# Performance work log

Hardware: AMD Instinct MI355X
Metric: run time of the kernel (lower is better)

## Reference

```python
import jax, jax.numpy as jnp
import numpy as np
from jax import lax

E = 18; I = 36; NH = 2; DHM = I // NH; DHS = E // NH; K = 4; S = 48; B = 4096
FF = 64  # multiple_of=64 rounding of 18*1.3

def _ln(x, w, eps=1e-5):
    mu = jnp.mean(x, axis=-1, keepdims=True)
    var = jnp.var(x, axis=-1, keepdims=True)
    return (x - mu) / jnp.sqrt(var + eps) * w

def _causal_conv(x, w, b):
    # x: (B,S,C); depthwise causal conv, w: (C,K), b: (C,)
    kk = w.shape[-1]
    xp = jnp.pad(x, ((0, 0), (kk - 1, 0), (0, 0)))
    y = lax.conv_general_dilated(xp, w[:, None, :], (1,), 'VALID',
                                 dimension_numbers=('NWC', 'OIW', 'NWC'),
                                 feature_group_count=x.shape[-1])
    return y + b

def _headwise(x, w):
    # block-diagonal linear (LinearHeadwiseExpand): w (n, dout, din)
    n, do, di = w.shape
    xr = x.reshape(x.shape[0], x.shape[1], n, di)
    return jnp.einsum('bsnd,nod->bsno', xr, w).reshape(x.shape[0], x.shape[1], n * do)

def _mlstm_parallel(q, k, v, ipre, fpre):
    # parallel_stabilized_simple: q,k,v (B,NH,S,DH); ipre,fpre (B,NH,S)
    dh = q.shape[-1]
    s = q.shape[2]
    lfc = jnp.cumsum(jax.nn.log_sigmoid(fpre), axis=-1)            # (B,NH,S)
    dlog = lfc[..., :, None] - lfc[..., None, :]                   # (B,NH,S,S): t,s
    mask = jnp.tril(jnp.ones((s, s), dtype=bool))
    logD = jnp.where(mask, dlog + ipre[..., None, :], -jnp.inf)
    maxD = jnp.max(logD, axis=-1, keepdims=True)
    D = jnp.exp(logD - maxD)
    qk = jnp.einsum('bhsd,bhtd->bhst', q, k * (dh ** -0.5))
    C = qk * D
    norm = jnp.maximum(jnp.abs(jnp.sum(C, axis=-1, keepdims=True)), jnp.exp(-maxD))
    return jnp.einsum('bhst,bhtd->bhsd', C / (norm + 1e-6), v)

def _mlstm_block(x, ln_w, up_w, cw, cb, qw, kw, vw, igw, igb, fgw, fgb, skip, onw, dw):
    bsz, s = x.shape[0], x.shape[1]
    h = _ln(x, ln_w)
    up = h @ up_w                                                  # (B,S,2I)
    xm, z = up[..., :I], up[..., I:]
    xc = jax.nn.silu(_causal_conv(xm, cw, cb))
    q = _headwise(xc, qw); k = _headwise(xc, kw); v = _headwise(xm, vw)
    gin = jnp.concatenate([q, k, v], axis=-1)                      # (B,S,3I)
    ipre = jnp.einsum('bsf,hf->bhs', gin, igw) + igb[None, :, None]
    fpre = jnp.einsum('bsf,hf->bhs', gin, fgw) + fgb[None, :, None]
    hd = lambda t: t.reshape(bsz, s, NH, DHM).transpose(0, 2, 1, 3)
    ht = _mlstm_parallel(hd(q), hd(k), hd(v), ipre, fpre)          # (B,NH,S,DHM)
    mu = jnp.mean(ht, axis=-1, keepdims=True)
    var = jnp.var(ht, axis=-1, keepdims=True)
    hn = (ht - mu) / jnp.sqrt(var + 1e-5) * onw.reshape(NH, DHM)[None, :, None, :]
    hn = hn.transpose(0, 2, 1, 3).reshape(bsz, s, I)
    hst = (hn + skip * xc) * jax.nn.silu(z)
    return x + hst @ dw

def _slstm_block(x, ln_w, cw, cb, gw, rw, gb, gnw, fln_w, fup_w, fdn_w):
    bsz, s = x.shape[0], x.shape[1]
    h = _ln(x, ln_w)
    hc = jax.nn.silu(_causal_conv(h, cw, cb))
    def gate(inp, w):
        return jnp.einsum('bsnd,nod->bsno', inp.reshape(bsz, s, NH, DHS), w)
    # gate order: i, f (from conv), z, o (from raw)
    wx = jnp.stack([gate(hc, gw[0]), gate(hc, gw[1]), gate(h, gw[2]), gate(h, gw[3])], axis=2)  # (B,S,4,NH,DHS)
    z0 = jnp.zeros((bsz, NH, DHS), x.dtype)
    def step(carry, wx_t):
        y, c, n, m = carry
        raw = wx_t + jnp.einsum('bhd,hdge->bghe', y, rw) + gb[None]  # (B,4,NH,DHS)
        i_, f_, z_, o_ = raw[:, 0], raw[:, 1], raw[:, 2], raw[:, 3]
        lfm = m + jax.nn.log_sigmoid(f_)
        mn = jnp.maximum(i_, lfm)
        ig = jnp.exp(i_ - mn)
        fg = jnp.exp(lfm - mn)
        cn = fg * c + ig * jnp.tanh(z_)
        nn = fg * n + ig
        yn = jax.nn.sigmoid(o_) * cn / nn
        return (yn, cn, nn, mn), yn
    _, ys = lax.scan(step, (z0, z0, z0, z0), wx.transpose(1, 0, 2, 3, 4))
    y = ys.transpose(1, 0, 2, 3)                                   # (B,S,NH,DHS)
    mu = jnp.mean(y, axis=-1, keepdims=True)
    var = jnp.var(y, axis=-1, keepdims=True)
    y = (y - mu) / jnp.sqrt(var + 1e-5) * gnw.reshape(NH, DHS)[None, None]
    x = x + y.reshape(bsz, s, E)
    h2 = _ln(x, fln_w)
    u = h2 @ fup_w                                                 # (B,S,2*FF)
    g, upp = u[..., :FF], u[..., FF:]
    return x + (jax.nn.gelu(g, approximate=False) * upp) @ fdn_w

def reference(x, m_ln_w, m_up_w, m_conv_w, m_conv_b, m_q_w, m_k_w, m_v_w,
              m_ig_w, m_ig_b, m_fg_w, m_fg_b, m_skip, m_on_w, m_down_w,
              s_ln_w, s_conv_w, s_conv_b, s_gate_w, s_rec_w, s_bias, s_gn_w,
              f_ln_w, f_up_w, f_down_w, post_ln_w, dense_w, dense_b):
    mj = 0
    for blk in range(7):
        if blk == 1:  # slstm_at=[1]
            x = _slstm_block(x, s_ln_w, s_conv_w, s_conv_b, s_gate_w, s_rec_w,
                             s_bias, s_gn_w, f_ln_w, f_up_w, f_down_w)
        else:
            x = _mlstm_block(x, m_ln_w[mj], m_up_w[mj], m_conv_w[mj], m_conv_b[mj],
                             m_q_w[mj], m_k_w[mj], m_v_w[mj], m_ig_w[mj], m_ig_b[mj],
                             m_fg_w[mj], m_fg_b[mj], m_skip[mj], m_on_w[mj], m_down_w[mj])
            mj += 1
    x = _ln(x, post_ln_w)
    out = x @ dense_w + dense_b
    return out.at[:, :24, :].set(0.0)

def setup_inputs():
    key = jax.random.key(0)
    ks = jax.random.split(key, 24)
    r = lambda i, shp, sc=0.1: jax.random.normal(ks[i], shp, dtype=jnp.float32) * sc
    return {
        'x': jax.random.normal(ks[0], (B, S, E), dtype=jnp.float32),
        'm_ln_w': jnp.ones((6, E), jnp.float32),
        'm_up_w': r(1, (6, E, 2 * I)),
        'm_conv_w': r(2, (6, I, K)),
        'm_conv_b': r(3, (6, I)),
        'm_q_w': r(4, (6, 9, 4, 4)),
        'm_k_w': r(5, (6, 9, 4, 4)),
        'm_v_w': r(6, (6, 9, 4, 4)),
        'm_ig_w': r(7, (6, NH, 3 * I)),
        'm_ig_b': r(8, (6, NH)),
        'm_fg_w': r(9, (6, NH, 3 * I)),
        'm_fg_b': r(10, (6, NH)),
        'm_skip': r(11, (6, I)),
        'm_on_w': jnp.ones((6, I), jnp.float32),
        'm_down_w': r(12, (6, I, E)),
        's_ln_w': jnp.ones((E,), jnp.float32),
        's_conv_w': r(13, (E, K)),
        's_conv_b': r(14, (E,)),
        's_gate_w': r(15, (4, NH, DHS, DHS)),
        's_rec_w': r(16, (NH, DHS, 4, DHS)),
        's_bias': r(17, (4, NH, DHS)),
        's_gn_w': jnp.ones((E,), jnp.float32),
        'f_ln_w': jnp.ones((E,), jnp.float32),
        'f_up_w': r(18, (E, 2 * FF)),
        'f_down_w': r(19, (FF, E)),
        'post_ln_w': jnp.ones((E,), jnp.float32),
        'dense_w': r(20, (E, 1)),
        'dense_b': r(21, (1,)),
    }
```

## Files before the change

### kernel.cpp

```cpp
#include <hip/hip_runtime.h>
#include <math.h>

#define TPB 256
#define WPB 4

constexpr int WAVE_F = 3552;
constexpr int O_SZ   = 2688;

constexpr int OW_UP  = 0;
constexpr int OW_AB  = 7776;
constexpr int OW_FUP = 9504;

__device__ __forceinline__ float sigm(float v){ return 1.f/(1.f+__expf(-v)); }
__device__ __forceinline__ float siluf(float v){ return v/(1.f+__expf(-v)); }
__device__ __forceinline__ float logsig(float v){ return fminf(v,0.f) - log1pf(__expf(-fabsf(v))); }
__device__ __forceinline__ float sqf(float v){ return v*v; }
__device__ __forceinline__ unsigned short f2b(float v){
  union{float f; unsigned u;} c; c.f=v; unsigned u=c.u;
  return (unsigned short)((u + 0x7FFFu + ((u>>16)&1u))>>16);
}
__device__ __forceinline__ float b2f(unsigned short s){
  union{unsigned u; float f;} c; c.u=((unsigned)s)<<16; return c.f;
}
__device__ __forceinline__ float u2f(unsigned u){
  union{unsigned u; float f;} c; c.u=u; return c.f;
}
__device__ __forceinline__ unsigned packbf(float a, float b){
  return (unsigned)f2b(a) | ((unsigned)f2b(b)<<16);
}
__device__ __forceinline__ float dot4(const float4 a, const float4 b){
  return a.x*b.x+a.y*b.y+a.z*b.z+a.w*b.w;
}

struct V18 { float4 a,b,c,d; float2 e; };
struct V36 { float4 g0,g1,g2,g3,g4,g5,g6,g7,g8; };

template<int I> __device__ __forceinline__ float elc(const V18& v){
  if constexpr(I==0) return v.a.x; else if constexpr(I==1) return v.a.y;
  else if constexpr(I==2) return v.a.z; else if constexpr(I==3) return v.a.w;
  else if constexpr(I==4) return v.b.x; else if constexpr(I==5) return v.b.y;
  else if constexpr(I==6) return v.b.z; else if constexpr(I==7) return v.b.w;
  else if constexpr(I==8) return v.c.x; else if constexpr(I==9) return v.c.y;
  else if constexpr(I==10) return v.c.z; else if constexpr(I==11) return v.c.w;
  else if constexpr(I==12) return v.d.x; else if constexpr(I==13) return v.d.y;
  else if constexpr(I==14) return v.d.z; else if constexpr(I==15) return v.d.w;
  else if constexpr(I==16) return v.e.x; else return v.e.y;
}
template<int I> __device__ __forceinline__ void setv(V18& v, float x){
  if constexpr(I==0) v.a.x=x; else if constexpr(I==1) v.a.y=x;
  else if constexpr(I==2) v.a.z=x; else if constexpr(I==3) v.a.w=x;
  else if constexpr(I==4) v.b.x=x; else if constexpr(I==5) v.b.y=x;
  else if constexpr(I==6) v.b.z=x; else if constexpr(I==7) v.b.w=x;
  else if constexpr(I==8) v.c.x=x; else if constexpr(I==9) v.c.y=x;
  else if constexpr(I==10) v.c.z=x; else if constexpr(I==11) v.c.w=x;
  else if constexpr(I==12) v.d.x=x; else if constexpr(I==13) v.d.y=x;
  else if constexpr(I==14) v.d.z=x; else if constexpr(I==15) v.d.w=x;
  else if constexpr(I==16) v.e.x=x; else v.e.y=x;
}
template<int G> __device__ __forceinline__ float4& grp(V36& q){
  if constexpr(G==0) return q.g0; else if constexpr(G==1) return q.g1;
  else if constexpr(G==2) return q.g2; else if constexpr(G==3) return q.g3;
  else if constexpr(G==4) return q.g4; else if constexpr(G==5) return q.g5;
  else if constexpr(G==6) return q.g6; else if constexpr(G==7) return q.g7;
  else return q.g8;
}

__device__ __forceinline__ float dot18(const V18& h, const float* __restrict__ w){
  return h.a.x*w[0]+h.a.y*w[1]+h.a.z*w[2]+h.a.w*w[3]
       + h.b.x*w[4]+h.b.y*w[5]+h.b.z*w[6]+h.b.w*w[7]
       + h.c.x*w[8]+h.c.y*w[9]+h.c.z*w[10]+h.c.w*w[11]
       + h.d.x*w[12]+h.d.y*w[13]+h.d.z*w[14]+h.d.w*w[15]
       + h.e.x*w[16]+h.e.y*w[17];
}
__device__ __forceinline__ void axpy18(V18& x, float s, const float* __restrict__ w){
  x.a.x+=s*w[0];  x.a.y+=s*w[1];  x.a.z+=s*w[2];  x.a.w+=s*w[3];
  x.b.x+=s*w[4];  x.b.y+=s*w[5];  x.b.z+=s*w[6];  x.b.w+=s*w[7];
  x.c.x+=s*w[8];  x.c.y+=s*w[9];  x.c.z+=s*w[10]; x.c.w+=s*w[11];
  x.d.x+=s*w[12]; x.d.y+=s*w[13]; x.d.z+=s*w[14]; x.d.w+=s*w[15];
  x.e.x+=s*w[16]; x.e.y+=s*w[17];
}
template<int B> __device__ __forceinline__ float dot9(const V18& v, const float* __restrict__ w){
  return elc<B+0>(v)*w[0]+elc<B+1>(v)*w[1]+elc<B+2>(v)*w[2]+elc<B+3>(v)*w[3]
       + elc<B+4>(v)*w[4]+elc<B+5>(v)*w[5]+elc<B+6>(v)*w[6]+elc<B+7>(v)*w[7]
       + elc<B+8>(v)*w[8];
}

#define L18(M) M(0) M(1) M(2) M(3) M(4) M(5) M(6) M(7) M(8) M(9) M(10) M(11) M(12) M(13) M(14) M(15) M(16) M(17)
#define L9(M) M(0) M(1) M(2) M(3) M(4) M(5) M(6) M(7) M(8)

extern "C" __global__ void prep_kernel(
    const float* __restrict__ up,  const float* __restrict__ qw, const float* __restrict__ kw,
    const float* __restrict__ vw,  const float* __restrict__ igw,const float* __restrict__ fgw,
    const float* __restrict__ fup, float* __restrict__ W)
{
  const int tid = threadIdx.x;
  for (int i=tid;i<7776;i+=256){ int mj=i/1296, r=i%1296, o=r/18, d=r%18; W[OW_UP+i]=up[mj*1296+d*72+o]; }
  for (int i=tid;i<1728;i+=256){
    int mj=i/288, r=i%288, gh=r/72, w2=(r%72)/36, c=r%36;
    int g=gh>>1,h=gh&1,n=c>>2,d=c&3;
    const float* gwp=(g? fgw:igw)+mj*216+h*108;
    float val=0.f;
    if(w2==0){ for(int o=0;o<4;++o) val += qw[mj*144+n*16+o*4+d]*gwp[n*4+o] + kw[mj*144+n*16+o*4+d]*gwp[36+n*4+o]; }
    else     { for(int o=0;o<4;++o) val += vw[mj*144+n*16+o*4+d]*gwp[72+n*4+o]; }
    W[OW_AB+i]=val;
  }
  for (int i=tid;i<2304;i+=256){ int f=i/18, d=i%18; W[OW_FUP+i]=fup[d*128+f]; }
}

template<int G>
__device__ __forceinline__ void proj_g(const V18& h, V18& x, V36& q,
    float* kvrow, unsigned short* szrow, int lane,
    const float* __restrict__ wup, const float* __restrict__ wab,
    const float* __restrict__ cw,  const float* __restrict__ cb,
    const float* __restrict__ qw,  const float* __restrict__ kw, const float* __restrict__ vw,
    const float* __restrict__ skp, const float* __restrict__ dwn,
    float& gi0, float& gi1, float& gf0, float& gf1)
{
  constexpr int C0=4*G;
  float m0=dot18(h,wup+(C0+0)*18), m1=dot18(h,wup+(C0+1)*18),
        m2=dot18(h,wup+(C0+2)*18), m3=dot18(h,wup+(C0+3)*18);
  if(lane>=48){ m0=0.f;m1=0.f;m2=0.f;m3=0.f; }
  float c0,c1,c2,c3;
  { float p1=__shfl(m0,lane-1),p2=__shfl(m0,lane-2),p3=__shfl(m0,lane-3);
    c0=siluf(cb[C0+0]+p3*cw[(C0+0)*4]+p2*cw[(C0+0)*4+1]+p1*cw[(C0+0)*4+2]+m0*cw[(C0+0)*4+3]); }
  { float p1=__shfl(m1,lane-1),p2=__shfl(m1,lane-2),p3=__shfl(m1,lane-3);
    c1=siluf(cb[C0+1]+p3*cw[(C0+1)*4]+p2*cw[(C0+1)*4+1]+p1*cw[(C0+1)*4+2]+m1*cw[(C0+1)*4+3]); }
  { float p1=__shfl(m2,lane-1),p2=__shfl(m2,lane-2),p3=__shfl(m2,lane-3);
    c2=siluf(cb[C0+2]+p3*cw[(C0+2)*4]+p2*cw[(C0+2)*4+1]+p1*cw[(C0+2)*4+2]+m2*cw[(C0+2)*4+3]); }
  { float p1=__shfl(m3,lane-1),p2=__shfl(m3,lane-2),p3=__shfl(m3,lane-3);
    c3=siluf(cb[C0+3]+p3*cw[(C0+3)*4]+p2*cw[(C0+3)*4+1]+p1*cw[(C0+3)*4+2]+m3*cw[(C0+3)*4+3]); }
  const float s0=siluf(dot18(h,wup+(36+C0+0)*18));
  const float s1=siluf(dot18(h,wup+(36+C0+1)*18));
  const float s2=siluf(dot18(h,wup+(36+C0+2)*18));
  const float s3=siluf(dot18(h,wup+(36+C0+3)*18));
  gi0 += c0*wab[C0+0]+c1*wab[C0+1]+c2*wab[C0+2]+c3*wab[C0+3]
       + m0*wab[36+C0+0]+m1*wab[36+C0+1]+m2*wab[36+C0+2]+m3*wab[36+C0+3];
  gi1 += c0*wab[72+C0+0]+c1*wab[72+C0+1]+c2*wab[72+C0+2]+c3*wab[72+C0+3]
       + m0*wab[108+C0+0]+m1*wab[108+C0+1]+m2*wab[108+C0+2]+m3*wab[108+C0+3];
  gf0 += c0*wab[144+C0+0]+c1*wab[144+C0+1]+c2*wab[144+C0+2]+c3*wab[144+C0+3]
       + m0*wab[180+C0+0]+m1*wab[180+C0+1]+m2*wab[180+C0+2]+m3*wab[180+C0+3];
  gf1 += c0*wab[216+C0+0]+c1*wab[216+C0+1]+c2*wab[216+C0+2]+c3*wab[216+C0+3]
       + m0*wab[252+C0+0]+m1*wab[252+C0+1]+m2*wab[252+C0+2]+m3*wab[252+C0+3];
  if(lane<48){
    uint2 ss; ss.x=packbf(s0,s1); ss.y=packbf(s2,s3);
    *reinterpret_cast<uint2*>(reinterpret_cast<unsigned*>(szrow) + (C0>>1)) = ss;
    float4 kk;
    kk.x=c0*kw[G*16+0] +c1*kw[G*16+1] +c2*kw[G*16+2] +c3*kw[G*16+3];
    kk.y=c0*kw[G*16+4] +c1*kw[G*16+5] +c2*kw[G*16+6] +c3*kw[G*16+7];
    kk.z=c0*kw[G*16+8] +c1*kw[G*16+9] +c2*kw[G*16+10]+c3*kw[G*16+11];
    kk.w=c0*kw[G*16+12]+c1*kw[G*16+13]+c2*kw[G*16+14]+c3*kw[G*16+15];
    *reinterpret_cast<float4*>(kvrow + C0) = kk;
    float vt0=m0*vw[G*16+0] +m1*vw[G*16+1] +m2*vw[G*16+2] +m3*vw[G*16+3];
    float vt1=m0*vw[G*16+4] +m1*vw[G*16+5] +m2*vw[G*16+6] +m3*vw[G*16+7];
    float vt2=m0*vw[G*16+8] +m1*vw[G*16+9] +m2*vw[G*16+10]+m3*vw[G*16+11];
    float vt3=m0*vw[G*16+12]+m1*vw[G*16+13]+m2*vw[G*16+14]+m3*vw[G*16+15];
    unsigned* urow = reinterpret_cast<unsigned*>(kvrow);
    if constexpr(G<4){
      uint2 vv; vv.x=packbf(vt0,vt1); vv.y=packbf(vt2,vt3);
      *reinterpret_cast<uint2*>(urow + 36 + 2*G) = vv;
    } else if constexpr(G==4){
      urow[44] = packbf(vt0,vt1);
      urow[46] = packbf(vt2,vt3);
    } else {
      urow[37+2*G] = packbf(vt0,vt1);
      urow[38+2*G] = packbf(vt2,vt3);
    }
  }
  float4 qt;
  qt.x=c0*qw[G*16+0] +c1*qw[G*16+1] +c2*qw[G*16+2] +c3*qw[G*16+3];
  qt.y=c0*qw[G*16+4] +c1*qw[G*16+5] +c2*qw[G*16+6] +c3*qw[G*16+7];
  qt.z=c0*qw[G*16+8] +c1*qw[G*16+9] +c2*qw[G*16+10]+c3*qw[G*16+11];
  qt.w=c0*qw[G*16+12]+c1*qw[G*16+13]+c2*qw[G*16+14]+c3*qw[G*16+15];
  grp<G>(q)=qt;
  axpy18(x, skp[C0+0]*c0*s0, dwn+(C0+0)*18);
  axpy18(x, skp[C0+1]*c1*s1, dwn+(C0+1)*18);
  axpy18(x, skp[C0+2]*c2*s2, dwn+(C0+2)*18);
  axpy18(x, skp[C0+3]*c3*s3, dwn+(C0+3)*18);
}

#define UNP(u, lo, hi) const float lo = u2f((u)<<16); const float hi = u2f((u)&0xffff0000u);

template<int HH>
__device__ __forceinline__ void attn_fold(const V36& q, V18& x, int lane,
    const float* KV, const unsigned short* szrow,
    float ipt, float lf, float u,
    const float* __restrict__ onw, const float* __restrict__ dwn)
{
  V18 acc;
  { float4 z4{0.f,0.f,0.f,0.f}; acc.a=z4; acc.b=z4; acc.c=z4; acc.d=z4; acc.e.x=0.f; acc.e.y=0.f; }
  float rs=0.f;
  const float rb=-u;
  const float scl=0.23570226039551584f;
  for(int t=0;t<48;++t){
    const float ipx = __shfl(ipt, t);
    const float* r = KV + t*56;
    float qk;
    if constexpr(HH==0){
      const float4 k0=*reinterpret_cast<const float4*>(r);
      const float4 k1=*reinterpret_cast<const float4*>(r+4);
      const float4 k2=*reinterpret_cast<const float4*>(r+8);
      const float4 k3=*reinterpret_cast<const float4*>(r+12);
      const float2 k4=*reinterpret_cast<const float2*>(r+16);
      qk = dot4(k0,q.g0)+dot4(k1,q.g1)+dot4(k2,q.g2)+dot4(k3,q.g3)
         + k4.x*q.g4.x + k4.y*q.g4.y;
    } else {
      const float2 k0=*reinterpret_cast<const float2*>(r+18);
      const float2 k1=*reinterpret_cast<const float2*>(r+20);
      const float2 k2=*reinterpret_cast<const float2*>(r+22);
      const float2 k3=*reinterpret_cast<const float2*>(r+24);
      const float2 k4=*reinterpret_cast<const float2*>(r+26);
      const float2 k5=*reinterpret_cast<const float2*>(r+28);
      const float2 k6=*reinterpret_cast<const float2*>(r+30);
      const float2 k7=*reinterpret_cast<const float2*>(r+32);
      const float2 k8=*reinterpret_cast<const float2*>(r+34);
      qk = k0.x*q.g4.z + k0.y*q.g4.w
         + k1.x*q.g5.x + k1.y*q.g5.y + k2.x*q.g5.z + k2.y*q.g5.w
         + k3.x*q.g6.x + k3.y*q.g6.y + k4.x*q.g6.z + k4.y*q.g6.w
         + k5.x*q.g7.x + k5.y*q.g7.y + k6.x*q.g7.z + k6.y*q.g7.w
         + k7.x*q.g8.x + k7.y*q.g8.y + k8.x*q.g8.z + k8.y*q.g8.w;
    }
    const float e0=__expf(fminf(rb+ipx,0.f));
    const float cc = (t<=lane)? qk*scl*e0 : 0.f;
    rs+=cc;
    const unsigned* ur = reinterpret_cast<const unsigned*>(r);
    if constexpr(HH==0){
      const uint4 va=*reinterpret_cast<const uint4*>(ur+36);
      const uint4 vb=*reinterpret_cast<const uint4*>(ur+40);
      const unsigned vc=ur[44];
      UNP(va.x,v0,v1) UNP(va.y,v2,v3) UNP(va.z,v4,v5) UNP(va.w,v6,v7)
      UNP(vb.x,v8,v9) UNP(vb.y,v10,v11) UNP(vb.z,v12,v13) UNP(vb.w,v14,v15)
      UNP(vc,v16,v17)
      acc.a.x+=cc*v0;  acc.a.y+=cc*v1;  acc.a.z+=cc*v2;  acc.a.w+=cc*v3;
      acc.b.x+=cc*v4;  acc.b.y+=cc*v5;  acc.b.z+=cc*v6;  acc.b.w+=cc*v7;
      acc.c.x+=cc*v8;  acc.c.y+=cc*v9;  acc.c.z+=cc*v10; acc.c.w+=cc*v11;
      acc.d.x+=cc*v12; acc.d.y+=cc*v13; acc.d.z+=cc*v14; acc.d.w+=cc*v15;
      acc.e.x+=cc*v16; acc.e.y+=cc*v17;
    } else {
      const uint2 w0=*reinterpret_cast<const uint2*>(ur+46);
      const uint4 w1=*reinterpret_cast<const uint4*>(ur+48);
      const uint2 w2=*reinterpret_cast<const uint2*>(ur+52);
      const unsigned w3=ur[54];
      UNP(w0.x,v0,v1) UNP(w0.y,v2,v3) UNP(w1.x,v4,v5) UNP(w1.y,v6,v7)
      UNP(w1.z,v8,v9) UNP(w1.w,v10,v11) UNP(w2.x,v12,v13) UNP(w2.y,v14,v15)
      UNP(w3,v16,v17)
      acc.a.x+=cc*v0;  acc.a.y+=cc*v1;  acc.a.z+=cc*v2;  acc.a.w+=cc*v3;
      acc.b.x+=cc*v4;  acc.b.y+=cc*v5;  acc.b.z+=cc*v6;  acc.b.w+=cc*v7;
      acc.c.x+=cc*v8;  acc.c.y+=cc*v9;  acc.c.z+=cc*v10; acc.c.w+=cc*v11;
      acc.d.x+=cc*v12; acc.d.y+=cc*v13; acc.d.z+=cc*v14; acc.d.w+=cc*v15;
      acc.e.x+=cc*v16; acc.e.y+=cc*v17;
    }
  }
  const float mr = lf+u;
  const float ninv = 1.f/(fmaxf(fabsf(rs), __expf(-mr))+1e-6f);
  #define AS(I) + elc<I>(acc)
  const float mb = (0.f L18(AS))*(1.f/18.f);
  #undef AS
  #define AV(I) + sqf(elc<I>(acc)-mb)
  const float vb2 = 0.f L18(AV);
  #undef AV
  const float rn = rsqrtf(ninv*ninv*vb2*(1.f/18.f)+1e-5f);
  #define FD(I) { const float hn=(elc<I>(acc)-mb)*ninv*rn*onw[HH*18+I]; \
                  axpy18(x, hn*b2f(szrow[HH*18+I]), dwn+(HH*18+I)*18); }
  L18(FD)
  #undef FD
}

__device__ __forceinline__ void mlstm(V18& x, int lane, float* WV, unsigned short* SZB,
    const float* __restrict__ lnw, const float* __restrict__ wup, const float* __restrict__ wab,
    const float* __restrict__ cw,  const float* __restrict__ cb,
    const float* __restrict__ qw,  const float* __restrict__ kw,  const float* __restrict__ vw,
    const float* __restrict__ igb, const float* __restrict__ fgb, const float* __restrict__ skp,
    const float* __restrict__ onw, const float* __restrict__ dwn)
{
  #define MS(I) + elc<I>(x)
  const float mu = (0.f L18(MS))*(1.f/18.f);
  #undef MS
  #define MV(I) + sqf(elc<I>(x)-mu)
  const float var = (0.f L18(MV))*(1.f/18.f);
  #undef MV
  const float rr = rsqrtf(var+1e-5f);
  V18 h;
  #define MH(I) setv<I>(h,(elc<I>(x)-mu)*rr*lnw[I]);
  L18(MH)
  #undef MH

  V36 q;
  float gi0=igb[0], gi1=igb[1], gf0=fgb[0], gf1=fgb[1];
  float* kvrow = WV + lane*56;
  const int sr = (lane<48)? lane : 0;
  unsigned short* szrow = SZB + sr*36;
  proj_g<0>(h,x,q,kvrow,szrow,lane,wup,wab,cw,cb,qw,kw,vw,skp,dwn,gi0,gi1,gf0,gf1);
  proj_g<1>(h,x,q,kvrow,szrow,lane,wup,wab,cw,cb,qw,kw,vw,skp,dwn,gi0,gi1,gf0,gf1);
  proj_g<2>(h,x,q,kvrow,szrow,lane,wup,wab,cw,cb,qw,kw,vw,skp,dwn,gi0,gi1,gf0,gf1);
  proj_g<3>(h,x,q,kvrow,szrow,lane,wup,wab,cw,cb,qw,kw,vw,skp,dwn,gi0,gi1,gf0,gf1);
  proj_g<4>(h,x,q,kvrow,szrow,lane,wup,wab,cw,cb,qw,kw,vw,skp,dwn,gi0,gi1,gf0,gf1);
  proj_g<5>(h,x,q,kvrow,szrow,lane,wup,wab,cw,cb,qw,kw,vw,skp,dwn,gi0,gi1,gf0,gf1);
  proj_g<6>(h,x,q,kvrow,szrow,lane,wup,wab,cw,cb,qw,kw,vw,skp,dwn,gi0,gi1,gf0,gf1);
  proj_g<7>(h,x,q,kvrow,szrow,lane,wup,wab,cw,cb,qw,kw,vw,skp,dwn,gi0,gi1,gf0,gf1);
  proj_g<8>(h,x,q,kvrow,szrow,lane,wup,wab,cw,cb,qw,kw,vw,skp,dwn,gi0,gi1,gf0,gf1);

  float lf0=logsig(gf0), lf1=logsig(gf1);
  #pragma unroll
  for(int off=1; off<64; off<<=1){
    float t0=__shfl_up(lf0,off), t1=__shfl_up(lf1,off);
    if(lane>=off){ lf0+=t0; lf1+=t1; }
  }
  const float ipt0=gi0-lf0, ipt1=gi1-lf1;
  float u0=ipt0, u1=ipt1;
  #pragma unroll
  for(int off=1; off<64; off<<=1){
    float t0=__shfl_up(u0,off), t1=__shfl_up(u1,off);
    if(lane>=off){ u0=fmaxf(u0,t0); u1=fmaxf(u1,t1); }
  }
  asm volatile("s_waitcnt lgkmcnt(0)" ::: "memory");

  attn_fold<0>(q, x, lane, WV, szrow, ipt0, lf0, u0, onw, dwn);
  attn_fold<1>(q, x, lane, WV, szrow, ipt1, lf1, u1, onw, dwn);
}

template<int IDX> __device__ __forceinline__ float wx1(const V18& h, const V18& hc,
    const float* __restrict__ gw, const float* __restrict__ gb){
  constexpr int g=IDX/18, hh=(IDX%18)/9;
  constexpr int B=hh*9;
  const float* w = gw + IDX*9;
  float a = gb[IDX];
  if constexpr(g<2) a += dot9<B>(hc,w); else a += dot9<B>(h,w);
  return a;
}
template<int Q4> __device__ __forceinline__ void wx4(const V18& h, const V18& hc,
    const float* __restrict__ gw, const float* __restrict__ gb, float* kvrow, int lane){
  float4 t;
  t.x=wx1<4*Q4+0>(h,hc,gw,gb);
  t.y=wx1<4*Q4+1>(h,hc,gw,gb);
  t.z=wx1<4*Q4+2>(h,hc,gw,gb);
  t.w=wx1<4*Q4+3>(h,hc,gw,gb);
  if(lane<48) *reinterpret_cast<float4*>(kvrow+4*Q4)=t;
}

__device__ __forceinline__ void slstm(V18& x, int lane, float* KV,
    const float* __restrict__ lnw, const float* __restrict__ cw, const float* __restrict__ cb,
    const float* __restrict__ gw,  const float* __restrict__ rw, const float* __restrict__ gb,
    const float* __restrict__ gnw, const float* __restrict__ flnw,
    const float* __restrict__ wfup,const float* __restrict__ fdw)
{
  #define SS(I) + elc<I>(x)
  const float mu = (0.f L18(SS))*(1.f/18.f);
  #undef SS
  #define SV(I) + sqf(elc<I>(x)-mu)
  const float var = (0.f L18(SV))*(1.f/18.f);
  #undef SV
  const float rr = rsqrtf(var+1e-5f);
  V18 h;
  #define SH(I) setv<I>(h,(lane<48)?(elc<I>(x)-mu)*rr*lnw[I]:0.f);
  L18(SH)
  #undef SH
  V18 hc;
  #define SC(I) { const float hv=elc<I>(h); \
    const float p1=__shfl(hv,lane-1),p2=__shfl(hv,lane-2),p3=__shfl(hv,lane-3); \
    setv<I>(hc, siluf(cb[I]+p3*cw[(I)*4]+p2*cw[(I)*4+1]+p1*cw[(I)*4+2]+hv*cw[(I)*4+3])); }
  L18(SC)
  #undef SC

  float* kvrow = KV + lane*72;
  wx4<0>(h,hc,gw,gb,kvrow,lane);  wx4<1>(h,hc,gw,gb,kvrow,lane);
  wx4<2>(h,hc,gw,gb,kvrow,lane);  wx4<3>(h,hc,gw,gb,kvrow,lane);
  wx4<4>(h,hc,gw,gb,kvrow,lane);  wx4<5>(h,hc,gw,gb,kvrow,lane);
  wx4<6>(h,hc,gw,gb,kvrow,lane);  wx4<7>(h,hc,gw,gb,kvrow,lane);
  wx4<8>(h,hc,gw,gb,kvrow,lane);  wx4<9>(h,hc,gw,gb,kvrow,lane);
  wx4<10>(h,hc,gw,gb,kvrow,lane); wx4<11>(h,hc,gw,gb,kvrow,lane);
  wx4<12>(h,hc,gw,gb,kvrow,lane); wx4<13>(h,hc,gw,gb,kvrow,lane);
  wx4<14>(h,hc,gw,gb,kvrow,lane); wx4<15>(h,hc,gw,gb,kvrow,lane);
  wx4<16>(h,hc,gw,gb,kvrow,lane); wx4<17>(h,hc,gw,gb,kvrow,lane);
  asm volatile("s_waitcnt lgkmcnt(0)" ::: "memory");

  for(int hh=0;hh<2;++hh){
    const int li = (lane<36)? lane : 0;
    const int g=li/9, e=li%9;
    const float* rwb = rw + hh*324 + g*9 + e;
    const float r0=rwb[0], r1=rwb[36], r2=rwb[72], r3=rwb[108], r4=rwb[144],
                r5=rwb[180], r6=rwb[216], r7=rwb[252], r8=rwb[288];
    float yv=0.f,cv=0.f,nv=0.f,mv=0.f;
    for(int st=0;st<48;++st){
      float raw = KV[st*72 + g*18 + hh*9 + e];
      raw += __shfl(yv,0)*r0 + __shfl(yv,1)*r1 + __shfl(yv,2)*r2
           + __shfl(yv,3)*r3 + __shfl(yv,4)*r4 + __shfl(yv,5)*r5
           + __shfl(yv,6)*r6 + __shfl(yv,7)*r7 + __shfl(yv,8)*r8;
      const float i_=__shfl(raw,e), f_=__shfl(raw,9+e), z_=__shfl(raw,18+e), o_=__shfl(raw,27+e);
      const float lfm=mv+logsig(f_);
      const float mn=fmaxf(i_,lfm);
      const float ig=__expf(i_-mn), fg=__expf(lfm-mn);
      const float th=1.f-2.f/(__expf(2.f*z_)+1.f);
      cv=fg*cv+ig*th;
      nv=fg*nv+ig; mv=mn;
      yv=sigm(o_)*cv/nv;
      if(lane<9) KV[st*72+hh*9+lane]=yv;
    }
  }
  asm volatile("s_waitcnt lgkmcnt(0)" ::: "memory");

  if(lane<48){
    {
      float m2=0.f;
      for(int e=0;e<9;++e) m2+=KV[lane*72+e];
      m2*=(1.f/9.f);
      float vv=0.f;
      for(int e=0;e<9;++e){ float t=KV[lane*72+e]-m2; vv+=t*t; }
      const float r2=rsqrtf(vv*(1.f/9.f)+1e-5f);
      #define GN0(E) setv<E>(x, elc<E>(x)+(KV[lane*72+E]-m2)*r2*gnw[E]);
      L9(GN0)
      #undef GN0
    }
    {
      float m2=0.f;
      for(int e=0;e<9;++e) m2+=KV[lane*72+9+e];
      m2*=(1.f/9.f);
      float vv=0.f;
      for(int e=0;e<9;++e){ float t=KV[lane*72+9+e]-m2; vv+=t*t; }
      const float r2=rsqrtf(vv*(1.f/9.f)+1e-5f);
      #define GN1(E) setv<(9+E)>(x, elc<(9+E)>(x)+(KV[lane*72+9+E]-m2)*r2*gnw[9+E]);
      L9(GN1)
      #undef GN1
    }
  }

  #define FS(I) + elc<I>(x)
  const float mu2 = (0.f L18(FS))*(1.f/18.f);
  #undef FS
  #define FV(I) + sqf(elc<I>(x)-mu2)
  const float var2 = (0.f L18(FV))*(1.f/18.f);
  #undef FV
  const float rr2 = rsqrtf(var2+1e-5f);
  V18 h2;
  #define FH(I) setv<I>(h2,(elc<I>(x)-mu2)*rr2*flnw[I]);
  L18(FH)
  #undef FH
  for(int f=0;f<64;++f){
    const float ug=dot18(h2, wfup+f*18);
    const float uu=dot18(h2, wfup+(64+f)*18);
    const float ge=0.5f*ug*(1.f+erff(ug*0.70710678118654752f));
    axpy18(x, ge*uu, fdw+f*18);
  }
}

extern "C" __global__ void __launch_bounds__(TPB)
xlstm_kernel(const float* __restrict__ gx,
             const float* __restrict__ m_ln_w,  const float* __restrict__ m_conv_w,
             const float* __restrict__ m_conv_b,const float* __restrict__ m_q_w,
             const float* __restrict__ m_k_w,   const float* __restrict__ m_v_w,
             const float* __restrict__ m_ig_b,  const float* __restrict__ m_fg_b,
             const float* __restrict__ m_skip,  const float* __restrict__ m_on_w,
             const float* __restrict__ m_down_w,
             const float* __restrict__ s_ln_w,  const float* __restrict__ s_conv_w,
             const float* __restrict__ s_conv_b,const float* __restrict__ s_gate_w,
             const float* __restrict__ s_rec_w, const float* __restrict__ s_bias,
             const float* __restrict__ s_gn_w,  const float* __restrict__ f_ln_w,
             const float* __restrict__ f_down_w,
             const float* __restrict__ post_ln_w, const float* __restrict__ dense_w,
             const float* __restrict__ dense_b, const float* __restrict__ W,
             float* __restrict__ gout, const int Btot)
{
  __shared__ float L[WPB*WAVE_F];
  const int lane = threadIdx.x & 63;
  const int wv   = threadIdx.x >> 6;
  const int b    = blockIdx.x*WPB + wv;
  if (b >= Btot) return;
  float* WV = L + wv*WAVE_F;
  unsigned short* SZB = reinterpret_cast<unsigned short*>(WV + O_SZ);

  V18 x;
  const float* gxb = gx + b*864 + lane*18;
  #define XL(I) setv<I>(x,(lane<48)? gxb[I] : 0.f);
  L18(XL)
  #undef XL

  int mj=0;
  #pragma unroll 1
  for(int blk=0; blk<7; ++blk){
    if (blk==1){
      slstm(x, lane, WV, s_ln_w, s_conv_w, s_conv_b, s_gate_w, s_rec_w, s_bias,
            s_gn_w, f_ln_w, W+OW_FUP, f_down_w);
    } else {
      mlstm(x, lane, WV, SZB,
            m_ln_w+mj*18, W+OW_UP+mj*1296, W+OW_AB+mj*288,
            m_conv_w+mj*144, m_conv_b+mj*36,
            m_q_w+mj*144, m_k_w+mj*144, m_v_w+mj*144,
            m_ig_b+mj*2, m_fg_b+mj*2, m_skip+mj*36, m_on_w+mj*36,
            m_down_w+mj*648);
      ++mj;
    }
  }

  if (lane<48){
    #define OS(I) + elc<I>(x)
    const float mu = (0.f L18(OS))*(1.f/18.f);
    #undef OS
    #define OV(I) + sqf(elc<I>(x)-mu)
    const float var = (0.f L18(OV))*(1.f/18.f);
    #undef OV
    const float rr = rsqrtf(var+1e-5f);
    float acc = dense_b[0];
    #define OD(I) acc += (elc<I>(x)-mu)*rr*post_ln_w[I]*dense_w[I];
    L18(OD)
    #undef OD
    gout[b*48+lane] = (lane<24) ? 0.f : acc;
  }
}

extern "C" void kernel_launch(void* const* d_in, const int* in_sizes, int n_in,
                              void* d_out, int out_size, void* d_ws, size_t ws_size,
                              hipStream_t stream)
{
  const float* gx        = (const float*)d_in[0];
  const float* m_ln_w    = (const float*)d_in[1];
  const float* m_up_w    = (const float*)d_in[2];
  const float* m_conv_w  = (const float*)d_in[3];
  const float* m_conv_b  = (const float*)d_in[4];
  const float* m_q_w     = (const float*)d_in[5];
  const float* m_k_w     = (const float*)d_in[6];
  const float* m_v_w     = (const float*)d_in[7];
  const float* m_ig_w    = (const float*)d_in[8];
  const float* m_ig_b    = (const float*)d_in[9];
  const float* m_fg_w    = (const float*)d_in[10];
  const float* m_fg_b    = (const float*)d_in[11];
  const float* m_skip    = (const float*)d_in[12];
  const float* m_on_w    = (const float*)d_in[13];
  const float* m_down_w  = (const float*)d_in[14];
  const float* s_ln_w    = (const float*)d_in[15];
  const float* s_conv_w  = (const float*)d_in[16];
  const float* s_conv_b  = (const float*)d_in[17];
  const float* s_gate_w  = (const float*)d_in[18];
  const float* s_rec_w   = (const float*)d_in[19];
  const float* s_bias    = (const float*)d_in[20];
  const float* s_gn_w    = (const float*)d_in[21];
  const float* f_ln_w    = (const float*)d_in[22];
  const float* f_up_w    = (const float*)d_in[23];
  const float* f_down_w  = (const float*)d_in[24];
  const float* post_ln_w = (const float*)d_in[25];
  const float* dense_w   = (const float*)d_in[26];
  const float* dense_b   = (const float*)d_in[27];

  float* W = (float*)d_ws;
  const int B = in_sizes[0] / (48*18);

  prep_kernel<<<1, 256, 0, stream>>>(m_up_w, m_q_w, m_k_w, m_v_w, m_ig_w, m_fg_w,
                                     f_up_w, W);
  xlstm_kernel<<<(B+WPB-1)/WPB, TPB, 0, stream>>>(gx,
    m_ln_w, m_conv_w, m_conv_b, m_q_w, m_k_w, m_v_w,
    m_ig_b, m_fg_b, m_skip, m_on_w, m_down_w,
    s_ln_w, s_conv_w, s_conv_b, s_gate_w, s_rec_w, s_bias, s_gn_w,
    f_ln_w, f_down_w, post_ln_w, dense_w, dense_b, W, (float*)d_out, B);
}
```

Before: 1.053 ms.

## Store K in bf16, shrink per-wave LDS, fuse sLSTM input projection into scan

Keys are now packed to bf16 like values, which shrinks the per-row LDS stride from 56 to 38 floats. The sLSTM input projection is computed inside the recurrent scan through shuffles instead of being precomputed into a 72-float-per-row LDS buffer, so the scratch only holds the 18-wide outputs. The smaller per-wave LDS footprint allows five waves per block instead of four, aiming at higher occupancy. The risks are lower precision on keys and extra shuffle work on the serial scan's critical path.

Measured after the change: 2.380 ms. +126.0%, slower.

```diff
diff --git a/kernel.cpp b/kernel.cpp
--- a/kernel.cpp
+++ b/kernel.cpp
@@ -1,11 +1,11 @@
 #include <hip/hip_runtime.h>
 #include <math.h>
 
-#define TPB 256
-#define WPB 4
-
-constexpr int WAVE_F = 3552;
-constexpr int O_SZ   = 2688;
+#define TPB 320
+#define WPB 5
+
+constexpr int WAVE_F = 2688;
+constexpr int O_SZ   = 1824;
 
 constexpr int OW_UP  = 0;
 constexpr int OW_AB  = 7776;
@@ -27,9 +27,6 @@
 }
 __device__ __forceinline__ unsigned packbf(float a, float b){
   return (unsigned)f2b(a) | ((unsigned)f2b(b)<<16);
-}
-__device__ __forceinline__ float dot4(const float4 a, const float4 b){
-  return a.x*b.x+a.y*b.y+a.z*b.z+a.w*b.w;
 }
 
 struct V18 { float4 a,b,c,d; float2 e; };
@@ -78,11 +75,6 @@
   x.c.x+=s*w[8];  x.c.y+=s*w[9];  x.c.z+=s*w[10]; x.c.w+=s*w[11];
   x.d.x+=s*w[12]; x.d.y+=s*w[13]; x.d.z+=s*w[14]; x.d.w+=s*w[15];
   x.e.x+=s*w[16]; x.e.y+=s*w[17];
-}
-template<int B> __device__ __forceinline__ float dot9(const V18& v, const float* __restrict__ w){
-  return elc<B+0>(v)*w[0]+elc<B+1>(v)*w[1]+elc<B+2>(v)*w[2]+elc<B+3>(v)*w[3]
-       + elc<B+4>(v)*w[4]+elc<B+5>(v)*w[5]+elc<B+6>(v)*w[6]+elc<B+7>(v)*w[7]
-       + elc<B+8>(v)*w[8];
 }
 
 #define L18(M) M(0) M(1) M(2) M(3) M(4) M(5) M(6) M(7) M(8) M(9) M(10) M(11) M(12) M(13) M(14) M(15) M(16) M(17)
@@ -144,27 +136,19 @@
   if(lane<48){
     uint2 ss; ss.x=packbf(s0,s1); ss.y=packbf(s2,s3);
     *reinterpret_cast<uint2*>(reinterpret_cast<unsigned*>(szrow) + (C0>>1)) = ss;
-    float4 kk;
-    kk.x=c0*kw[G*16+0] +c1*kw[G*16+1] +c2*kw[G*16+2] +c3*kw[G*16+3];
-    kk.y=c0*kw[G*16+4] +c1*kw[G*16+5] +c2*kw[G*16+6] +c3*kw[G*16+7];
-    kk.z=c0*kw[G*16+8] +c1*kw[G*16+9] +c2*kw[G*16+10]+c3*kw[G*16+11];
-    kk.w=c0*kw[G*16+12]+c1*kw[G*16+13]+c2*kw[G*16+14]+c3*kw[G*16+15];
-    *reinterpret_cast<float4*>(kvrow + C0) = kk;
-    float vt0=m0*vw[G*16+0] +m1*vw[G*16+1] +m2*vw[G*16+2] +m3*vw[G*16+3];
-    float vt1=m0*vw[G*16+4] +m1*vw[G*16+5] +m2*vw[G*16+6] +m3*vw[G*16+7];
-    float vt2=m0*vw[G*16+8] +m1*vw[G*16+9] +m2*vw[G*16+10]+m3*vw[G*16+11];
-    float vt3=m0*vw[G*16+12]+m1*vw[G*16+13]+m2*vw[G*16+14]+m3*vw[G*16+15];
+    const float kt0=c0*kw[G*16+0] +c1*kw[G*16+1] +c2*kw[G*16+2] +c3*kw[G*16+3];
+    const float kt1=c0*kw[G*16+4] +c1*kw[G*16+5] +c2*kw[G*16+6] +c3*kw[G*16+7];
+    const float kt2=c0*kw[G*16+8] +c1*kw[G*16+9] +c2*kw[G*16+10]+c3*kw[G*16+11];
+    const float kt3=c0*kw[G*16+12]+c1*kw[G*16+13]+c2*kw[G*16+14]+c3*kw[G*16+15];
+    const float vt0=m0*vw[G*16+0] +m1*vw[G*16+1] +m2*vw[G*16+2] +m3*vw[G*16+3];
+    const float vt1=m0*vw[G*16+4] +m1*vw[G*16+5] +m2*vw[G*16+6] +m3*vw[G*16+7];
+    const float vt2=m0*vw[G*16+8] +m1*vw[G*16+9] +m2*vw[G*16+10]+m3*vw[G*16+11];
+    const float vt3=m0*vw[G*16+12]+m1*vw[G*16+13]+m2*vw[G*16+14]+m3*vw[G*16+15];
     unsigned* urow = reinterpret_cast<unsigned*>(kvrow);
-    if constexpr(G<4){
-      uint2 vv; vv.x=packbf(vt0,vt1); vv.y=packbf(vt2,vt3);
-      *reinterpret_cast<uint2*>(urow + 36 + 2*G) = vv;
-    } else if constexpr(G==4){
-      urow[44] = packbf(vt0,vt1);
-      urow[46] = packbf(vt2,vt3);
-    } else {
-      urow[37+2*G] = packbf(vt0,vt1);
-      urow[38+2*G] = packbf(vt2,vt3);
-    }
+    uint2 kk2; kk2.x=packbf(kt0,kt1); kk2.y=packbf(kt2,kt3);
+    *reinterpret_cast<uint2*>(urow + 2*G) = kk2;
+    uint2 vv2; vv2.x=packbf(vt0,vt1); vv2.y=packbf(vt2,vt3);
+    *reinterpret_cast<uint2*>(urow + 18 + 2*G) = vv2;
   }
   float4 qt;
   qt.x=c0*qw[G*16+0] +c1*qw[G*16+1] +c2*qw[G*16+2] +c3*qw[G*16+3];
@@ -193,56 +177,67 @@
   const float scl=0.23570226039551584f;
   for(int t=0;t<48;++t){
     const float ipx = __shfl(ipt, t);
-    const float* r = KV + t*56;
+    const unsigned* ur = reinterpret_cast<const unsigned*>(KV + t*38);
     float qk;
     if constexpr(HH==0){
-      const float4 k0=*reinterpret_cast<const float4*>(r);
-      const float4 k1=*reinterpret_cast<const float4*>(r+4);
-      const float4 k2=*reinterpret_cast<const float4*>(r+8);
-      const float4 k3=*reinterpret_cast<const float4*>(r+12);
-      const float2 k4=*reinterpret_cast<const float2*>(r+16);
-      qk = dot4(k0,q.g0)+dot4(k1,q.g1)+dot4(k2,q.g2)+dot4(k3,q.g3)
-         + k4.x*q.g4.x + k4.y*q.g4.y;
+      const uint2 a0=*reinterpret_cast<const uint2*>(ur+0);
+      const uint2 a1=*reinterpret_cast<const uint2*>(ur+2);
+      const uint2 a2=*reinterpret_cast<const uint2*>(ur+4);
+      const uint2 a3=*reinterpret_cast<const uint2*>(ur+6);
+      const unsigned a4=ur[8];
+      UNP(a0.x,k0,k1) UNP(a0.y,k2,k3) UNP(a1.x,k4,k5) UNP(a1.y,k6,k7)
+      UNP(a2.x,k8,k9) UNP(a2.y,k10,k11) UNP(a3.x,k12,k13) UNP(a3.y,k14,k15)
+      UNP(a4,k16,k17)
+      qk = k0*q.g0.x+k1*q.g0.y+k2*q.g0.z+k3*q.g0.w
+         + k4*q.g1.x+k5*q.g1.y+k6*q.g1.z+k7*q.g1.w
+         + k8*q.g2.x+k9*q.g2.y+k10*q.g2.z+k11*q.g2.w
+         + k12*q.g3.x+k13*q.g3.y+k14*q.g3.z+k15*q.g3.w
+         + k16*q.g4.x+k17*q.g4.y;
     } else {
-      const float2 k0=*reinterpret_cast<const float2*>(r+18);
-      const float2 k1=*reinterpret_cast<const float2*>(r+20);
-      const float2 k2=*reinterpret_cast<const float2*>(r+22);
-      const float2 k3=*reinterpret_cast<const float2*>(r+24);
-      const float2 k4=*reinterpret_cast<const float2*>(r+26);
-      const float2 k5=*reinterpret_cast<const float2*>(r+28);
-      const float2 k6=*reinterpret_cast<const float2*>(r+30);
-      const float2 k7=*reinterpret_cast<const float2*>(r+32);
-      const float2 k8=*reinterpret_cast<const float2*>(r+34);
-      qk = k0.x*q.g4.z + k0.y*q.g4.w
-         + k1.x*q.g5.x + k1.y*q.g5.y + k2.x*q.g5.z + k2.y*q.g5.w
-         + k3.x*q.g6.x + k3.y*q.g6.y + k4.x*q.g6.z + k4.y*q.g6.w
-         + k5.x*q.g7.x + k5.y*q.g7.y + k6.x*q.g7.z + k6.y*q.g7.w
-         + k7.x*q.g8.x + k7.y*q.g8.y + k8.x*q.g8.z + k8.y*q.g8.w;
+      const unsigned a0=ur[9];
+      const uint2 a1=*reinterpret_cast<const uint2*>(ur+10);
+      const uint2 a2=*reinterpret_cast<const uint2*>(ur+12);
+      const uint2 a3=*reinterpret_cast<const uint2*>(ur+14);
+      const uint2 a4=*reinterpret_cast<const uint2*>(ur+16);
+      UNP(a0,k18,k19)
+      UNP(a1.x,k20,k21) UNP(a1.y,k22,k23)
+      UNP(a2.x,k24,k25) UNP(a2.y,k26,k27)
+      UNP(a3.x,k28,k29) UNP(a3.y,k30,k31)
+      UNP(a4.x,k32,k33) UNP(a4.y,k34,k35)
+      qk = k18*q.g4.z+k19*q.g4.w
+         + k20*q.g5.x+k21*q.g5.y+k22*q.g5.z+k23*q.g5.w
+         + k24*q.g6.x+k25*q.g6.y+k26*q.g6.z+k27*q.g6.w
+         + k28*q.g7.x+k29*q.g7.y+k30*q.g7.z+k31*q.g7.w
+         + k32*q.g8.x+k33*q.g8.y+k34*q.g8.z+k35*q.g8.w;
     }
     const float e0=__expf(fminf(rb+ipx,0.f));
     const float cc = (t<=lane)? qk*scl*e0 : 0.f;
     rs+=cc;
-    const unsigned* ur = reinterpret_cast<const unsigned*>(r);
     if constexpr(HH==0){
-      const uint4 va=*reinterpret_cast<const uint4*>(ur+36);
-      const uint4 vb=*reinterpret_cast<const uint4*>(ur+40);
-      const unsigned vc=ur[44];
-      UNP(va.x,v0,v1) UNP(va.y,v2,v3) UNP(va.z,v4,v5) UNP(va.w,v6,v7)
-      UNP(vb.x,v8,v9) UNP(vb.y,v10,v11) UNP(vb.z,v12,v13) UNP(vb.w,v14,v15)
-      UNP(vc,v16,v17)
+      const uint2 b0=*reinterpret_cast<const uint2*>(ur+18);
+      const uint2 b1=*reinterpret_cast<const uint2*>(ur+20);
+      const uint2 b2=*reinterpret_cast<const uint2*>(ur+22);
+      const uint2 b3=*reinterpret_cast<const uint2*>(ur+24);
+      const unsigned b4=ur[26];
+      UNP(b0.x,v0,v1) UNP(b0.y,v2,v3) UNP(b1.x,v4,v5) UNP(b1.y,v6,v7)
+      UNP(b2.x,v8,v9) UNP(b2.y,v10,v11) UNP(b3.x,v12,v13) UNP(b3.y,v14,v15)
+      UNP(b4,v16,v17)
       acc.a.x+=cc*v0;  acc.a.y+=cc*v1;  acc.a.z+=cc*v2;  acc.a.w+=cc*v3;
       acc.b.x+=cc*v4;  acc.b.y+=cc*v5;  acc.b.z+=cc*v6;  acc.b.w+=cc*v7;
       acc.c.x+=cc*v8;  acc.c.y+=cc*v9;  acc.c.z+=cc*v10; acc.c.w+=cc*v11;
       acc.d.x+=cc*v12; acc.d.y+=cc*v13; acc.d.z+=cc*v14; acc.d.w+=cc*v15;
       acc.e.x+=cc*v16; acc.e.y+=cc*v17;
     } else {
-      const uint2 w0=*reinterpret_cast<const uint2*>(ur+46);
-      const uint4 w1=*reinterpret_cast<const uint4*>(ur+48);
-      const uint2 w2=*reinterpret_cast<const uint2*>(ur+52);
-      const unsigned w3=ur[54];
-      UNP(w0.x,v0,v1) UNP(w0.y,v2,v3) UNP(w1.x,v4,v5) UNP(w1.y,v6,v7)
-      UNP(w1.z,v8,v9) UNP(w1.w,v10,v11) UNP(w2.x,v12,v13) UNP(w2.y,v14,v15)
-      UNP(w3,v16,v17)
+      const unsigned b0=ur[27];
+      const uint2 b1=*reinterpret_cast<const uint2*>(ur+28);
+      const uint2 b2=*reinterpret_cast<const uint2*>(ur+30);
+      const uint2 b3=*reinterpret_cast<const uint2*>(ur+32);
+      const uint2 b4=*reinterpret_cast<const uint2*>(ur+34);
+      UNP(b0,v0,v1)
+      UNP(b1.x,v2,v3) UNP(b1.y,v4,v5)
+      UNP(b2.x,v6,v7) UNP(b2.y,v8,v9)
+      UNP(b3.x,v10,v11) UNP(b3.y,v12,v13)
+      UNP(b4.x,v14,v15) UNP(b4.y,v16,v17)
       acc.a.x+=cc*v0;  acc.a.y+=cc*v1;  acc.a.z+=cc*v2;  acc.a.w+=cc*v3;
       acc.b.x+=cc*v4;  acc.b.y+=cc*v5;  acc.b.z+=cc*v6;  acc.b.w+=cc*v7;
       acc.c.x+=cc*v8;  acc.c.y+=cc*v9;  acc.c.z+=cc*v10; acc.c.w+=cc*v11;
@@ -286,7 +281,7 @@
 
   V36 q;
   float gi0=igb[0], gi1=igb[1], gf0=fgb[0], gf1=fgb[1];
-  float* kvrow = WV + lane*56;
+  float* kvrow = WV + lane*38;
   const int sr = (lane<48)? lane : 0;
   unsigned short* szrow = SZB + sr*36;
   proj_g<0>(h,x,q,kvrow,szrow,lane,wup,wab,cw,cb,qw,kw,vw,skp,dwn,gi0,gi1,gf0,gf1);
@@ -318,26 +313,44 @@
   attn_fold<1>(q, x, lane, WV, szrow, ipt1, lf1, u1, onw, dwn);
 }
 
-template<int IDX> __device__ __forceinline__ float wx1(const V18& h, const V18& hc,
-    const float* __restrict__ gw, const float* __restrict__ gb){
-  constexpr int g=IDX/18, hh=(IDX%18)/9;
-  constexpr int B=hh*9;
-  const float* w = gw + IDX*9;
-  float a = gb[IDX];
-  if constexpr(g<2) a += dot9<B>(hc,w); else a += dot9<B>(h,w);
-  return a;
-}
-template<int Q4> __device__ __forceinline__ void wx4(const V18& h, const V18& hc,
-    const float* __restrict__ gw, const float* __restrict__ gb, float* kvrow, int lane){
-  float4 t;
-  t.x=wx1<4*Q4+0>(h,hc,gw,gb);
-  t.y=wx1<4*Q4+1>(h,hc,gw,gb);
-  t.z=wx1<4*Q4+2>(h,hc,gw,gb);
-  t.w=wx1<4*Q4+3>(h,hc,gw,gb);
-  if(lane<48) *reinterpret_cast<float4*>(kvrow+4*Q4)=t;
-}
-
-__device__ __forceinline__ void slstm(V18& x, int lane, float* KV,
+template<int HH>
+__device__ __forceinline__ void scan_head(const V18& h, const V18& hc, int lane, float* Y,
+    const float* __restrict__ gw, const float* __restrict__ gb, const float* __restrict__ rw)
+{
+  const int li = (lane<36)? lane : 0;
+  const int g=li/9, e=li%9;
+  const float* gwb = gw + ((g*2+HH)*9+e)*9;
+  const float w0=gwb[0],w1=gwb[1],w2=gwb[2],w3=gwb[3],w4=gwb[4],
+              w5=gwb[5],w6=gwb[6],w7=gwb[7],w8=gwb[8];
+  const float bias = gb[(g*2+HH)*9+e];
+  const float* rwb = rw + HH*324 + g*9 + e;
+  const float r0=rwb[0], r1=rwb[36], r2=rwb[72], r3=rwb[108], r4=rwb[144],
+              r5=rwb[180], r6=rwb[216], r7=rwb[252], r8=rwb[288];
+  const bool usehc = (g<2);
+  float yv=0.f,cv=0.f,nv=0.f,mv=0.f;
+  for(int st=0; st<48; ++st){
+    float raw = bias;
+    #define BIN(D,W) { const float bh=__shfl(elc<9*HH+D>(h),st); \
+                       const float bc=__shfl(elc<9*HH+D>(hc),st); \
+                       raw += (usehc? bc : bh)*W; }
+    BIN(0,w0) BIN(1,w1) BIN(2,w2) BIN(3,w3) BIN(4,w4) BIN(5,w5) BIN(6,w6) BIN(7,w7) BIN(8,w8)
+    #undef BIN
+    raw += __shfl(yv,0)*r0 + __shfl(yv,1)*r1 + __shfl(yv,2)*r2
+         + __shfl(yv,3)*r3 + __shfl(yv,4)*r4 + __shfl(yv,5)*r5
+         + __shfl(yv,6)*r6 + __shfl(yv,7)*r7 + __shfl(yv,8)*r8;
+    const float i_=__shfl(raw,e), f_=__shfl(raw,9+e), z_=__shfl(raw,18+e), o_=__shfl(raw,27+e);
+    const float lfm=mv+logsig(f_);
+    const float mn=fmaxf(i_,lfm);
+    const float ig=__expf(i_-mn), fg=__expf(lfm-mn);
+    const float th=1.f-2.f/(__expf(2.f*z_)+1.f);
+    cv=fg*cv+ig*th;
+    nv=fg*nv+ig; mv=mn;
+    yv=sigm(o_)*cv/nv;
+    if(lane<9) Y[st*18 + HH*9 + lane] = yv;
+  }
+}
+
+__device__ __forceinline__ void slstm(V18& x, int lane, float* Y,
     const float* __restrict__ lnw, const float* __restrict__ cw, const float* __restrict__ cb,
     const float* __restrict__ gw,  const float* __restrict__ rw, const float* __restrict__ gb,
     const float* __restrict__ gnw, const float* __restrict__ flnw,
@@ -361,63 +374,30 @@
   L18(SC)
   #undef SC
 
-  float* kvrow = KV + lane*72;
-  wx4<0>(h,hc,gw,gb,kvrow,lane);  wx4<1>(h,hc,gw,gb,kvrow,lane);
-  wx4<2>(h,hc,gw,gb,kvrow,lane);  wx4<3>(h,hc,gw,gb,kvrow,lane);
-  wx4<4>(h,hc,gw,gb,kvrow,lane);  wx4<5>(h,hc,gw,gb,kvrow,lane);
-  wx4<6>(h,hc,gw,gb,kvrow,lane);  wx4<7>(h,hc,gw,gb,kvrow,lane);
-  wx4<8>(h,hc,gw,gb,kvrow,lane);  wx4<9>(h,hc,gw,gb,kvrow,lane);
-  wx4<10>(h,hc,gw,gb,kvrow,lane); wx4<11>(h,hc,gw,gb,kvrow,lane);
-  wx4<12>(h,hc,gw,gb,kvrow,lane); wx4<13>(h,hc,gw,gb,kvrow,lane);
-  wx4<14>(h,hc,gw,gb,kvrow,lane); wx4<15>(h,hc,gw,gb,kvrow,lane);
-  wx4<16>(h,hc,gw,gb,kvrow,lane); wx4<17>(h,hc,gw,gb,kvrow,lane);
-  asm volatile("s_waitcnt lgkmcnt(0)" ::: "memory");
-
-  for(int hh=0;hh<2;++hh){
-    const int li = (lane<36)? lane : 0;
-    const int g=li/9, e=li%9;
-    const float* rwb = rw + hh*324 + g*9 + e;
-    const float r0=rwb[0], r1=rwb[36], r2=rwb[72], r3=rwb[108], r4=rwb[144],
-                r5=rwb[180], r6=rwb[216], r7=rwb[252], r8=rwb[288];
-    float yv=0.f,cv=0.f,nv=0.f,mv=0.f;
-    for(int st=0;st<48;++st){
-      float raw = KV[st*72 + g*18 + hh*9 + e];
-      raw += __shfl(yv,0)*r0 + __shfl(yv,1)*r1 + __shfl(yv,2)*r2
-           + __shfl(yv,3)*r3 + __shfl(yv,4)*r4 + __shfl(yv,5)*r5
-           + __shfl(yv,6)*r6 + __shfl(yv,7)*r7 + __shfl(yv,8)*r8;
-      const float i_=__shfl(raw,e), f_=__shfl(raw,9+e), z_=__shfl(raw,18+e), o_=__shfl(raw,27+e);
-      const float lfm=mv+logsig(f_);
-      const float mn=fmaxf(i_,lfm);
-      const float ig=__expf(i_-mn), fg=__expf(lfm-mn);
-      const float th=1.f-2.f/(__expf(2.f*z_)+1.f);
-      cv=fg*cv+ig*th;
-      nv=fg*nv+ig; mv=mn;
-      yv=sigm(o_)*cv/nv;
-      if(lane<9) KV[st*72+hh*9+lane]=yv;
-    }
-  }
+  scan_head<0>(h, hc, lane, Y, gw, gb, rw);
+  scan_head<1>(h, hc, lane, Y, gw, gb, rw);
   asm volatile("s_waitcnt lgkmcnt(0)" ::: "memory");
 
   if(lane<48){
     {
       float m2=0.f;
-      for(int e=0;e<9;++e) m2+=KV[lane*72+e];
+      for(int e=0;e<9;++e) m2+=Y[lane*18+e];
       m2*=(1.f/9.f);
       float vv=0.f;
-      for(int e=0;e<9;++e){ float t=KV[lane*72+e]-m2; vv+=t*t; }
+      for(int e=0;e<9;++e){ float t=Y[lane*18+e]-m2; vv+=t*t; }
       const float r2=rsqrtf(vv*(1.f/9.f)+1e-5f);
-      #define GN0(E) setv<E>(x, elc<E>(x)+(KV[lane*72+E]-m2)*r2*gnw[E]);
+      #define GN0(E) setv<E>(x, elc<E>(x)+(Y[lane*18+E]-m2)*r2*gnw[E]);
       L9(GN0)
       #undef GN0
     }
     {
       float m2=0.f;
-      for(int e=0;e<9;++e) m2+=KV[lane*72+9+e];
+      for(int e=0;e<9;++e) m2+=Y[lane*18+9+e];
       m2*=(1.f/9.f);
       float vv=0.f;
-      for(int e=0;e<9;++e){ float t=KV[lane*72+9+e]-m2; vv+=t*t; }
+      for(int e=0;e<9;++e){ float t=Y[lane*18+9+e]-m2; vv+=t*t; }
       const float r2=rsqrtf(vv*(1.f/9.f)+1e-5f);
-      #define GN1(E) setv<(9+E)>(x, elc<(9+E)>(x)+(KV[lane*72+9+E]-m2)*r2*gnw[9+E]);
+      #define GN1(E) setv<(9+E)>(x, elc<(9+E)>(x)+(Y[lane*18+9+E]-m2)*r2*gnw[9+E]);
       L9(GN1)
       #undef GN1
     }
```
